# Kernel optimization log

Hardware: AMD Instinct MI355X
Metric: run time of the kernel (lower is better)

## Reference

```python
import jax, jax.numpy as jnp
import numpy as np

H = 768  # hidden size
L = 2    # num layers


def _lstm_layer(xs, ms, Wih, Whh, bih, bhh):
    """xs: [S,B,in], ms: [S,B,H] mask. Returns (outputs [S,B,H], (hT, cT)).
    PyTorch LSTMCell gate order: i, f, g, o. Zero initial state (module default),
    so the reset term init_hidden*(1-mask) is identically zero."""
    B = xs.shape[1]
    h0 = jnp.zeros((B, H), xs.dtype)
    c0 = jnp.zeros((B, H), xs.dtype)
    # Precompute input projections for all timesteps in one big GEMM.
    x_proj = jnp.einsum('sbi,gi->sbg', xs, Wih) + bih + bhh  # [S,B,4H]

    def step(carry, inp):
        h, c = carry
        xp, mt = inp
        gates = xp + h @ Whh.T  # [B,4H]
        i, f, g, o = jnp.split(gates, 4, axis=-1)
        i = jax.nn.sigmoid(i)
        f = jax.nn.sigmoid(f)
        g = jnp.tanh(g)
        o = jax.nn.sigmoid(o)
        c_next = (f * c + i * g)
        h_next = o * jnp.tanh(c_next)
        # mask-based state reset (h0=c0=0 -> pure multiply)
        h_next = h_next * mt
        c_next = c_next * mt
        return (h_next, c_next), h_next

    (hT, cT), outs = jax.lax.scan(step, (h0, c0), (x_proj, ms))
    return outs, (hT, cT)


def setup_inputs() -> dict:
    key = jax.random.key(0)
    ks = jax.random.split(key, 5)
    s = 0.05
    return {
        'x': jax.random.normal(ks[0], (64, 512, 768), jnp.float32),
        'mask': jnp.ones((64, 512), jnp.float32),
        'W_ih': jax.random.normal(ks[1], (L, 4 * H, 768), jnp.float32) * s,
        'W_hh': jax.random.normal(ks[2], (L, 4 * H, H), jnp.float32) * s,
        'b_ih': jax.random.normal(ks[3], (L, 4 * H), jnp.float32) * s,
        'b_hh': jax.random.normal(ks[4], (L, 4 * H), jnp.float32) * s,
    }


def reference(x, mask, W_ih, W_hh, b_ih, b_hh):
    # batch_first=True: transpose to [S,B,...]
    xs = jnp.transpose(x, (1, 0, 2))          # [S,B,in]
    ms = jnp.transpose(mask, (1, 0))[:, :, None]  # [S,B,1]
    ms = jnp.broadcast_to(ms, ms.shape[:2] + (H,))  # [S,B,H]
    hn, cn = [], []
    inp = xs
    for l in range(L):
        outs, (hT, cT) = _lstm_layer(inp, ms, W_ih[l], W_hh[l], b_ih[l], b_hh[l])
        hn.append(hT)
        cn.append(cT)
        inp = outs
    output = jnp.transpose(inp, (1, 0, 2))  # [B,S,H]
    return output, (jnp.stack(hn, 0), jnp.stack(cn, 0))
```

## Files before the change

### kernel.cpp

```cpp
#include <hip/hip_runtime.h>
#include <hip/hip_bf16.h>


#define HID 768
#define FH  3072
#define SEQ 512
#define BAT 64
#define GB  16
#define WPG 64
#define NWG 256
#define TPB 1024

typedef __attribute__((ext_vector_type(8))) __bf16 bf16x8;
typedef __attribute__((ext_vector_type(4))) float f32x4;
typedef unsigned int u32;
typedef unsigned long long u64;

__device__ __forceinline__ float sigm(float z) { return 1.f / (1.f + __expf(-z)); }
__device__ __forceinline__ float tanh_fast(float x) {
  float a = fabsf(x);
  float e = __expf(-2.f * a);
  float t = (1.f - e) / (1.f + e);
  return copysignf(t, x);
}
__device__ __forceinline__ unsigned short bfbits(__bf16 b) {
  union { __bf16 b; unsigned short s; } u; u.b = b; return u.s;
}
__device__ __forceinline__ __bf16 bits2bf(unsigned short s) {
  union { unsigned short s; __bf16 b; } u; u.s = s; return u.b;
}
__device__ __forceinline__ u32 packsplit(float v) {
  __bf16 h = (__bf16)v;
  __bf16 l = (__bf16)(v - (float)h);
  return ((u32)bfbits(h) << 16) | (u32)bfbits(l);
}
__device__ __forceinline__ void split8(const float* p, bf16x8& hi, bf16x8& lo) {
  const float4* q = (const float4*)p;
  float4 a = q[0], b = q[1];
  float v[8] = {a.x, a.y, a.z, a.w, b.x, b.y, b.z, b.w};
#pragma unroll
  for (int i = 0; i < 8; ++i) {
    __bf16 h = (__bf16)v[i];
    hi[i] = h;
    lo[i] = (__bf16)(v[i] - (float)h);
  }
}
__device__ __forceinline__ void unpack8(const u32 w[8], bf16x8& hi, bf16x8& lo) {
#pragma unroll
  for (int i = 0; i < 8; ++i) {
    hi[i] = bits2bf((unsigned short)(w[i] >> 16));
    lo[i] = bits2bf((unsigned short)(w[i] & 0xffffu));
  }
}
__device__ __forceinline__ bf16x8 q2b(uint4 q) {
  union { uint4 q; bf16x8 v; } u; u.q = q; return u.v;
}
__device__ __forceinline__ uint4 b2q(bf16x8 v) {
  union { bf16x8 v; uint4 q; } u; u.v = v; return u.q;
}

__global__ void pack_w(const float* __restrict__ Wih,
                       const float* __restrict__ Whh,
                       u32* __restrict__ wpk) {
  int g = blockIdx.x * blockDim.x + threadIdx.x;
  const int NT = 2 * 9216 * 64;
  if (g >= NT) return;
  int lane = g & 63;
  int sl = g >> 6;
  int region = sl / 9216;
  int sr = sl % 9216;
  int l15 = lane & 15, lhi = lane >> 4;
  int k, t, wid, layer;
  const float* W;
  if (region == 0) {
    int c  = sr % 8;
    t      = (sr / 8) % 3;
    int xw = (sr / 24) % 3;
    wid    = (sr / 72) % 64;
    layer  = sr / 4608;
    k = xw*256 + c*32 + lhi*8;
    W = Wih + (size_t)layer*FH*HID;
  } else {
    int c  = sr % 2;
    t      = (sr / 2) % 3;
    int j  = (sr / 6) % 12;
    wid    = (sr / 72) % 64;
    layer  = sr / 4608;
    k = j*64 + c*32 + lhi*8;
    W = Whh + (size_t)layer*FH*HID;
  }
  int row = (l15 & 3)*HID + wid*12 + t*4 + (l15 >> 2);
  bf16x8 hi, lo;
  split8(W + (size_t)row*HID + k, hi, lo);
  u32* dst = wpk + ((size_t)region*9216 + sr)*512 + lane*8;
  *(uint4*)dst       = b2q(hi);
  *(uint4*)(dst + 4) = b2q(lo);
}

#define MFMA16 __builtin_amdgcn_mfma_f32_16x16x32_bf16

template<int XFMT, int WRITE_OUT, int RING>
__attribute__((amdgpu_waves_per_eu(4, 4)))
__global__ void __launch_bounds__(TPB)
lstm_scan(const float* __restrict__ xf,
          const u32* __restrict__ xp,
          const float* __restrict__ mask,
          const u32* __restrict__ wipk,
          const u32* __restrict__ whpk,
          const float* __restrict__ bih,
          const float* __restrict__ bhh,
          u32* __restrict__ hdst,
          const u32* __restrict__ hsrc,
          float* __restrict__ out_f,
          float* __restrict__ hn, float* __restrict__ cn,
          int* __restrict__ flags)
{
  __shared__ f32x4 xring[4][3][3][64];
  __shared__ f32x4 hpart[12][3][64];
  __shared__ f32x4 padlds[512];

  const int wg  = blockIdx.x;
  const int grp = wg >> 6;
  const int wid = wg & 63;
  const int tid = threadIdx.x;
  const int wv  = tid >> 6;
  const int l   = tid & 63;
  const int l15 = l & 15;
  const int lhi = l >> 4;

  if ((int)blockIdx.x == -1) padlds[tid & 511] = hpart[0][0][0];

  const bool ish  = (wv < 12);
  const bool isxw = (wv >= 12 && wv < 15);
  const int j  = wv;
  const int xw = wv - 12;

  const int batch = grp*GB + l15;
  const u32* wbj = whpk + (size_t)(wid*12 + (ish  ? j  : 0))*6*512;
  const u32* wbx = wipk + (size_t)(wid*3  + (isxw ? xw : 0))*24*512;

  const int colO = wid*12 + (isxw ? xw : 0)*4 + lhi;
  float bias4[4] = {0.f, 0.f, 0.f, 0.f};
  if (isxw) {
#pragma unroll
    for (int r = 0; r < 4; ++r) bias4[r] = bih[r*HID + colO] + bhh[r*HID + colO];
  }
  const float* mrow = mask + batch*SEQ;
  int* gflags = flags + grp*WPG;
  float cstate = 0.f;

  auto xproj = [&](int sstep, int slot) {
    f32x4 a0{0.f,0.f,0.f,0.f}, a1{0.f,0.f,0.f,0.f}, a2{0.f,0.f,0.f,0.f};
#pragma unroll
    for (int c = 0; c < 8; ++c) {
      bf16x8 bhi, blo;
      if constexpr (XFMT == 0) {
        const float* src = xf + ((size_t)batch*SEQ + sstep)*HID + xw*256 + c*32 + lhi*8;
        split8(src, bhi, blo);
      } else {
        const u32* src = xp + ((size_t)sstep*BAT + batch)*HID + xw*256 + c*32 + lhi*8;
        uint4 A = *(const uint4*)src, B = *(const uint4*)(src + 4);
        u32 w[8] = {A.x,A.y,A.z,A.w,B.x,B.y,B.z,B.w};
        unpack8(w, bhi, blo);
      }
      {
        const uint4* wp = (const uint4*)(wbx + (size_t)(0*8 + c)*512 + l*8);
        bf16x8 Ah = q2b(wp[0]), Al = q2b(wp[1]);
        a0 = MFMA16(Ah, bhi, a0, 0,0,0); a0 = MFMA16(Al, bhi, a0, 0,0,0); a0 = MFMA16(Ah, blo, a0, 0,0,0);
      }
      {
        const uint4* wp = (const uint4*)(wbx + (size_t)(1*8 + c)*512 + l*8);
        bf16x8 Ah = q2b(wp[0]), Al = q2b(wp[1]);
        a1 = MFMA16(Ah, bhi, a1, 0,0,0); a1 = MFMA16(Al, bhi, a1, 0,0,0); a1 = MFMA16(Ah, blo, a1, 0,0,0);
      }
      {
        const uint4* wp = (const uint4*)(wbx + (size_t)(2*8 + c)*512 + l*8);
        bf16x8 Ah = q2b(wp[0]), Al = q2b(wp[1]);
        a2 = MFMA16(Ah, bhi, a2, 0,0,0); a2 = MFMA16(Al, bhi, a2, 0,0,0); a2 = MFMA16(Ah, blo, a2, 0,0,0);
      }
    }
    xring[slot][xw][0][l] = a0;
    xring[slot][xw][1][l] = a1;
    xring[slot][xw][2][l] = a2;
  };

  if (isxw) xproj(0, 0);
  __syncthreads();

#pragma unroll 1
  for (int s = 0; s < SEQ; ++s) {
    if (wv == 15 && s > 0) {
      while (true) {
        int v = __hip_atomic_load(gflags + l, __ATOMIC_RELAXED, __HIP_MEMORY_SCOPE_AGENT);
        if (__all(v >= s)) break;
        __builtin_amdgcn_s_sleep(1);
      }
    }
    __syncthreads();

    if (ish && s > 0) {
      f32x4 a0{0.f,0.f,0.f,0.f}, a1{0.f,0.f,0.f,0.f}, a2{0.f,0.f,0.f,0.f};
#pragma unroll
      for (int c = 0; c < 2; ++c) {
        u32 w[8];
        if constexpr (RING) {
          const u64* sp = (const u64*)(hsrc + ((size_t)((s-1)&1)*BAT + batch)*HID + j*64 + c*32 + lhi*8);
          u64 qa = __hip_atomic_load(sp,   __ATOMIC_RELAXED, __HIP_MEMORY_SCOPE_AGENT);
          u64 qb = __hip_atomic_load(sp+1, __ATOMIC_RELAXED, __HIP_MEMORY_SCOPE_AGENT);
          u64 qc = __hip_atomic_load(sp+2, __ATOMIC_RELAXED, __HIP_MEMORY_SCOPE_AGENT);
          u64 qd = __hip_atomic_load(sp+3, __ATOMIC_RELAXED, __HIP_MEMORY_SCOPE_AGENT);
          w[0]=(u32)qa; w[1]=(u32)(qa>>32); w[2]=(u32)qb; w[3]=(u32)(qb>>32);
          w[4]=(u32)qc; w[5]=(u32)(qc>>32); w[6]=(u32)qd; w[7]=(u32)(qd>>32);
        } else {
          const u32* sp = hsrc + ((size_t)(s-1)*BAT + batch)*HID + j*64 + c*32 + lhi*8;
          uint4 A = *(const uint4*)sp, B = *(const uint4*)(sp + 4);
          w[0]=A.x; w[1]=A.y; w[2]=A.z; w[3]=A.w;
          w[4]=B.x; w[5]=B.y; w[6]=B.z; w[7]=B.w;
        }
        bf16x8 bhi, blo;
        unpack8(w, bhi, blo);
        {
          const uint4* wp = (const uint4*)(wbj + (size_t)(0*2 + c)*512 + l*8);
          bf16x8 Ah = q2b(wp[0]), Al = q2b(wp[1]);
          a0 = MFMA16(Ah, bhi, a0, 0,0,0); a0 = MFMA16(Al, bhi, a0, 0,0,0); a0 = MFMA16(Ah, blo, a0, 0,0,0);
        }
        {
          const uint4* wp = (const uint4*)(wbj + (size_t)(1*2 + c)*512 + l*8);
          bf16x8 Ah = q2b(wp[0]), Al = q2b(wp[1]);
          a1 = MFMA16(Ah, bhi, a1, 0,0,0); a1 = MFMA16(Al, bhi, a1, 0,0,0); a1 = MFMA16(Ah, blo, a1, 0,0,0);
        }
        {
          const uint4* wp = (const uint4*)(wbj + (size_t)(2*2 + c)*512 + l*8);
          bf16x8 Ah = q2b(wp[0]), Al = q2b(wp[1]);
          a2 = MFMA16(Ah, bhi, a2, 0,0,0); a2 = MFMA16(Al, bhi, a2, 0,0,0); a2 = MFMA16(Ah, blo, a2, 0,0,0);
        }
      }
      hpart[j][0][l] = a0;
      hpart[j][1][l] = a1;
      hpart[j][2][l] = a2;
    }
    if (isxw && s + 1 < SEQ) xproj(s + 1, (s + 1) & 3);
    __syncthreads();

    if (isxw) {
      f32x4 z = xring[s & 3][0][xw][l] + xring[s & 3][1][xw][l] + xring[s & 3][2][xw][l];
      if (s > 0) {
#pragma unroll
        for (int jj = 0; jj < 12; ++jj) z = z + hpart[jj][xw][l];
      }
      float zi = z[0] + bias4[0], zf = z[1] + bias4[1];
      float zg = z[2] + bias4[2], zo = z[3] + bias4[3];
      float iv = sigm(zi), fv = sigm(zf), gv = tanh_fast(zg), ov = sigm(zo);
      float c  = fv*cstate + iv*gv;
      float hv = ov * tanh_fast(c);
      float m  = mrow[s];
      hv *= m; c *= m; cstate = c;

      u32 hw = packsplit(hv);
      size_t wrow = RING ? ((size_t)(s & 1)*BAT + batch)*HID + colO
                         : ((size_t)s*BAT + batch)*HID + colO;
      __hip_atomic_store(hdst + wrow, hw,
                         __ATOMIC_RELAXED, __HIP_MEMORY_SCOPE_AGENT);
      if constexpr (WRITE_OUT) {
        __builtin_nontemporal_store(hv, out_f + ((size_t)batch*SEQ + s)*HID + colO);
      }
      if (s == SEQ - 1) {
        hn[batch*HID + colO] = hv;
        cn[batch*HID + colO] = c;
      }
      asm volatile("s_waitcnt vmcnt(0)" ::: "memory");
    }
    __syncthreads();
    if (tid == 0)
      __hip_atomic_store(gflags + wid, s + 1,
                         __ATOMIC_RELAXED, __HIP_MEMORY_SCOPE_AGENT);
  }
}

extern "C" void kernel_launch(void* const* d_in, const int* in_sizes, int n_in,
                              void* d_out, int out_size, void* d_ws, size_t ws_size,
                              hipStream_t stream) {
  const float* x    = (const float*)d_in[0];
  const float* mask = (const float*)d_in[1];
  const float* Wih  = (const float*)d_in[2];
  const float* Whh  = (const float*)d_in[3];
  const float* bih  = (const float*)d_in[4];
  const float* bhh  = (const float*)d_in[5];
  float* out = (float*)d_out;

  char* ws = (char*)d_ws;
  const size_t WPK_B   = (size_t)2*9216*512*4;
  const size_t STREAM_B = (size_t)SEQ*BAT*HID*4;
  const size_t RING_B  = (size_t)2*BAT*HID*4;

  u32* wpk = (u32*)ws;
  u32* opk = (u32*)(ws + WPK_B);
  const bool big = ws_size >= WPK_B + 2*STREAM_B + 4096;
  u32* h1  = (u32*)(ws + WPK_B + STREAM_B);
  int* flags = big ? (int*)(ws + WPK_B + 2*STREAM_B)
                   : (int*)(ws + WPK_B + STREAM_B + RING_B);

  (void)hipMemsetAsync(flags, 0, 2*NWG*sizeof(int), stream);
  pack_w<<<4608, 256, 0, stream>>>(Wih, Whh, wpk);

  float* hn = out + 25165824;
  float* cn = out + 25165824 + 98304;

  const u32* wipk0 = wpk;
  const u32* wipk1 = wpk + (size_t)4608*512;
  const u32* whpk0 = wpk + (size_t)9216*512;
  const u32* whpk1 = wpk + (size_t)13824*512;

  lstm_scan<0, 0, 0><<<dim3(NWG), dim3(TPB), 0, stream>>>(
      x, nullptr, mask, wipk0, whpk0, bih, bhh,
      opk, opk, nullptr, hn, cn, flags);

  if (big) {
    lstm_scan<1, 1, 0><<<dim3(NWG), dim3(TPB), 0, stream>>>(
        nullptr, opk, mask, wipk1, whpk1, bih + FH, bhh + FH,
        h1, h1, out, hn + 49152, cn + 49152, flags + NWG);
  } else {
    lstm_scan<1, 1, 1><<<dim3(NWG), dim3(TPB), 0, stream>>>(
        nullptr, opk, mask, wipk1, whpk1, bih + FH, bhh + FH,
        h1, h1, out, hn + 49152, cn + 49152, flags + NWG);
  }
}
```

Measured before the change: 13.76 ms.

## Replace flag-poll barrier with per-step arrival counters polled by hidden waves

The old scheme had a dedicated wave poll 64 per-workgroup flags, then ran a block barrier at the top of every timestep, and published progress after a second barrier. Now each group keeps a per-timestep global counter that the three gate-writing waves bump through an LDS tally. Only the recurrent-matmul waves spin on the previous step's counter, which removes one block barrier per step and its fan-in latency. hpart is double-buffered and the input projection is prefetched two steps ahead so the gate waves can overlap with the next step's recurrent work. The cost is more LDS, a larger zeroed counter array, and more delicate ordering, especially in the two-slot ring mode.

```diff
diff --git a/kernel.cpp b/kernel.cpp
--- a/kernel.cpp
+++ b/kernel.cpp
@@ -7,7 +7,6 @@
 #define SEQ 512
 #define BAT 64
 #define GB  16
-#define WPG 64
 #define NWG 256
 #define TPB 1024
 
@@ -70,11 +69,10 @@
   int region = sl / 9216;
   int sr = sl % 9216;
   int l15 = lane & 15, lhi = lane >> 4;
-  int k, t, wid, layer;
+  int k, wid, layer;
   const float* W;
   if (region == 0) {
     int c  = sr % 8;
-    t      = (sr / 8) % 3;
     int xw = (sr / 24) % 3;
     wid    = (sr / 72) % 64;
     layer  = sr / 4608;
@@ -82,13 +80,13 @@
     W = Wih + (size_t)layer*FH*HID;
   } else {
     int c  = sr % 2;
-    t      = (sr / 2) % 3;
     int j  = (sr / 6) % 12;
     wid    = (sr / 72) % 64;
     layer  = sr / 4608;
     k = j*64 + c*32 + lhi*8;
     W = Whh + (size_t)layer*FH*HID;
   }
+  int t = (region == 0) ? (sr / 8) % 3 : (sr / 2) % 3;
   int row = (l15 & 3)*HID + wid*12 + t*4 + (l15 >> 2);
   bf16x8 hi, lo;
   split8(W + (size_t)row*HID + k, hi, lo);
@@ -113,11 +111,11 @@
           const u32* __restrict__ hsrc,
           float* __restrict__ out_f,
           float* __restrict__ hn, float* __restrict__ cn,
-          int* __restrict__ flags)
+          int* __restrict__ cnt)
 {
   __shared__ f32x4 xring[4][3][3][64];
-  __shared__ f32x4 hpart[12][3][64];
-  __shared__ f32x4 padlds[512];
+  __shared__ f32x4 hpart[2][12][3][64];
+  __shared__ int   lfin[SEQ];
 
   const int wg  = blockIdx.x;
   const int grp = wg >> 6;
@@ -128,8 +126,6 @@
   const int l15 = l & 15;
   const int lhi = l >> 4;
 
-  if ((int)blockIdx.x == -1) padlds[tid & 511] = hpart[0][0][0];
-
   const bool ish  = (wv < 12);
   const bool isxw = (wv >= 12 && wv < 15);
   const int j  = wv;
@@ -146,8 +142,10 @@
     for (int r = 0; r < 4; ++r) bias4[r] = bih[r*HID + colO] + bhh[r*HID + colO];
   }
   const float* mrow = mask + batch*SEQ;
-  int* gflags = flags + grp*WPG;
+  int* gcnt = cnt + grp*SEQ;
   float cstate = 0.f;
+
+  for (int i = tid; i < SEQ; i += TPB) lfin[i] = 0;
 
   auto xproj = [&](int sstep, int slot) {
     f32x4 a0{0.f,0.f,0.f,0.f}, a1{0.f,0.f,0.f,0.f}, a2{0.f,0.f,0.f,0.f};
@@ -184,21 +182,14 @@
     xring[slot][xw][2][l] = a2;
   };
 
-  if (isxw) xproj(0, 0);
-  __syncthreads();
+  if (isxw) { xproj(0, 0); xproj(1, 1); }
 
 #pragma unroll 1
   for (int s = 0; s < SEQ; ++s) {
-    if (wv == 15 && s > 0) {
-      while (true) {
-        int v = __hip_atomic_load(gflags + l, __ATOMIC_RELAXED, __HIP_MEMORY_SCOPE_AGENT);
-        if (__all(v >= s)) break;
-        __builtin_amdgcn_s_sleep(1);
-      }
-    }
-    __syncthreads();
-
     if (ish && s > 0) {
+      const int* cp = gcnt + (s - 1);
+      while (__hip_atomic_load(cp, __ATOMIC_RELAXED, __HIP_MEMORY_SCOPE_AGENT) < 64)
+        __builtin_amdgcn_s_sleep(2);
       f32x4 a0{0.f,0.f,0.f,0.f}, a1{0.f,0.f,0.f,0.f}, a2{0.f,0.f,0.f,0.f};
 #pragma unroll
       for (int c = 0; c < 2; ++c) {
@@ -235,18 +226,18 @@
           a2 = MFMA16(Ah, bhi, a2, 0,0,0); a2 = MFMA16(Al, bhi, a2, 0,0,0); a2 = MFMA16(Ah, blo, a2, 0,0,0);
         }
       }
-      hpart[j][0][l] = a0;
-      hpart[j][1][l] = a1;
-      hpart[j][2][l] = a2;
+      hpart[s & 1][j][0][l] = a0;
+      hpart[s & 1][j][1][l] = a1;
+      hpart[s & 1][j][2][l] = a2;
     }
-    if (isxw && s + 1 < SEQ) xproj(s + 1, (s + 1) & 3);
+    if (isxw && s + 2 < SEQ) xproj(s + 2, (s + 2) & 3);
     __syncthreads();
 
     if (isxw) {
       f32x4 z = xring[s & 3][0][xw][l] + xring[s & 3][1][xw][l] + xring[s & 3][2][xw][l];
       if (s > 0) {
 #pragma unroll
-        for (int jj = 0; jj < 12; ++jj) z = z + hpart[jj][xw][l];
+        for (int jj = 0; jj < 12; ++jj) z = z + hpart[s & 1][jj][xw][l];
       }
       float zi = z[0] + bias4[0], zf = z[1] + bias4[1];
       float zg = z[2] + bias4[2], zo = z[3] + bias4[3];
@@ -269,11 +260,13 @@
         cn[batch*HID + colO] = c;
       }
       asm volatile("s_waitcnt vmcnt(0)" ::: "memory");
+      if (l == 0) {
+        int old = atomicAdd(&lfin[s], 1);
+        if (old == 2)
+          __hip_atomic_fetch_add(gcnt + s, 1,
+                                 __ATOMIC_RELAXED, __HIP_MEMORY_SCOPE_AGENT);
+      }
     }
-    __syncthreads();
-    if (tid == 0)
-      __hip_atomic_store(gflags + wid, s + 1,
-                         __ATOMIC_RELAXED, __HIP_MEMORY_SCOPE_AGENT);
   }
 }
 
@@ -295,12 +288,12 @@
 
   u32* wpk = (u32*)ws;
   u32* opk = (u32*)(ws + WPK_B);
-  const bool big = ws_size >= WPK_B + 2*STREAM_B + 4096;
+  const bool big = ws_size >= WPK_B + 2*STREAM_B + 65536;
   u32* h1  = (u32*)(ws + WPK_B + STREAM_B);
-  int* flags = big ? (int*)(ws + WPK_B + 2*STREAM_B)
-                   : (int*)(ws + WPK_B + STREAM_B + RING_B);
-
-  (void)hipMemsetAsync(flags, 0, 2*NWG*sizeof(int), stream);
+  int* cnt = big ? (int*)(ws + WPK_B + 2*STREAM_B)
+                 : (int*)(ws + WPK_B + STREAM_B + RING_B);
+
+  (void)hipMemsetAsync(cnt, 0, 2*4*SEQ*sizeof(int), stream);
   pack_w<<<4608, 256, 0, stream>>>(Wih, Whh, wpk);
 
   float* hn = out + 25165824;
@@ -313,15 +306,15 @@
 
   lstm_scan<0, 0, 0><<<dim3(NWG), dim3(TPB), 0, stream>>>(
       x, nullptr, mask, wipk0, whpk0, bih, bhh,
-      opk, opk, nullptr, hn, cn, flags);
+      opk, opk, nullptr, hn, cn, cnt);
 
   if (big) {
     lstm_scan<1, 1, 0><<<dim3(NWG), dim3(TPB), 0, stream>>>(
         nullptr, opk, mask, wipk1, whpk1, bih + FH, bhh + FH,
-        h1, h1, out, hn + 49152, cn + 49152, flags + NWG);
+        h1, h1, out, hn + 49152, cn + 49152, cnt + 4*SEQ);
   } else {
     lstm_scan<1, 1, 1><<<dim3(NWG), dim3(TPB), 0, stream>>>(
         nullptr, opk, mask, wipk1, whpk1, bih + FH, bhh + FH,
-        h1, h1, out, hn + 49152, cn + 49152, flags + NWG);
-  }
-}
+        h1, h1, out, hn + 49152, cn + 49152, cnt + 4*SEQ);
+  }
+}
```

Result: slower. 15.16 ms (+10.2%).

## Split input projection into segmented GEMM kernels and keep Whh in registers

Applied to the files above, without the earlier changes.

Moves the per-step input projection out of the persistent scan kernel into a separate batched GEMM over 64-step segments. The scan runs segment by segment and carries cell state through global memory between launches. Recurrent Whh fragments now stay in registers instead of being reloaded every step. Step completion is signalled per workgroup through an LDS counter instead of a block-wide barrier. The cost is 16 extra kernel launches and a round trip of the projection results through global memory, in exchange for a shorter serial critical path per step.

```diff
diff --git a/kernel.cpp b/kernel.cpp
--- a/kernel.cpp
+++ b/kernel.cpp
@@ -7,9 +7,11 @@
 #define SEQ 512
 #define BAT 64
 #define GB  16
-#define WPG 64
+#define SSEG 64
+#define SEGS 8
 #define NWG 256
-#define TPB 1024
+#define STPB 960
+#define GTPB 768
 
 typedef __attribute__((ext_vector_type(8))) __bf16 bf16x8;
 typedef __attribute__((ext_vector_type(4))) float f32x4;
@@ -33,6 +35,10 @@
   __bf16 h = (__bf16)v;
   __bf16 l = (__bf16)(v - (float)h);
   return ((u32)bfbits(h) << 16) | (u32)bfbits(l);
+}
+__device__ __forceinline__ float unpackf(u32 w) {
+  return (float)bits2bf((unsigned short)(w >> 16)) +
+         (float)bits2bf((unsigned short)(w & 0xffffu));
 }
 __device__ __forceinline__ void split8(const float* p, bf16x8& hi, bf16x8& lo) {
   const float4* q = (const float4*)p;
@@ -73,12 +79,12 @@
   int k, t, wid, layer;
   const float* W;
   if (region == 0) {
-    int c  = sr % 8;
-    t      = (sr / 8) % 3;
-    int xw = (sr / 24) % 3;
+    int c  = sr % 6;
+    int ks = (sr / 6) % 4;
+    t      = (sr / 24) % 3;
     wid    = (sr / 72) % 64;
     layer  = sr / 4608;
-    k = xw*256 + c*32 + lhi*8;
+    k = ks*192 + c*32 + lhi*8;
     W = Wih + (size_t)layer*FH*HID;
   } else {
     int c  = sr % 2;
@@ -99,25 +105,101 @@
 
 #define MFMA16 __builtin_amdgcn_mfma_f32_16x16x32_bf16
 
-template<int XFMT, int WRITE_OUT, int RING>
-__attribute__((amdgpu_waves_per_eu(4, 4)))
-__global__ void __launch_bounds__(TPB)
-lstm_scan(const float* __restrict__ xf,
-          const u32* __restrict__ xp,
+template<int XFMT>
+__global__ void __launch_bounds__(GTPB)
+xproj_gemm(const float* __restrict__ xf,
+           const u32* __restrict__ xp,
+           const u32* __restrict__ wih_pk,
+           u32* __restrict__ xpk,
+           int s0)
+{
+  __shared__ f32x4 part[3][4][4][64];
+
+  const int wg  = blockIdx.x;
+  const int sq  = wg & 3;
+  const int wid = (wg >> 2) & 63;
+  const int grp = wg >> 8;
+  const int tid = threadIdx.x;
+  const int wv  = tid >> 6;
+  const int l   = tid & 63;
+  const int l15 = l & 15;
+  const int lhi = l >> 4;
+  const int t   = wv >> 2;
+  const int ks  = wv & 3;
+
+  const int batch = grp*GB + l15;
+  const u32* wb = wih_pk + (((size_t)(wid*3 + t)*4 + ks)*6)*512;
+
+  uint4 wa[12];
+#pragma unroll
+  for (int c = 0; c < 6; ++c) {
+    const uint4* wp = (const uint4*)(wb + (size_t)c*512 + l*8);
+    wa[c*2]   = wp[0];
+    wa[c*2+1] = wp[1];
+  }
+
+#pragma unroll 1
+  for (int i0 = 0; i0 < 16; i0 += 4) {
+    f32x4 acc[4];
+#pragma unroll
+    for (int i = 0; i < 4; ++i) acc[i] = f32x4{0.f, 0.f, 0.f, 0.f};
+#pragma unroll
+    for (int c = 0; c < 6; ++c) {
+      int k = ks*192 + c*32 + lhi*8;
+      bf16x8 Ah = q2b(wa[c*2]), Al = q2b(wa[c*2+1]);
+#pragma unroll
+      for (int i = 0; i < 4; ++i) {
+        int sg = s0 + sq*16 + i0 + i;
+        bf16x8 bhi, blo;
+        if constexpr (XFMT == 0) {
+          split8(xf + ((size_t)batch*SEQ + sg)*HID + k, bhi, blo);
+        } else {
+          const u32* sp = xp + ((size_t)sg*BAT + batch)*HID + k;
+          uint4 A = *(const uint4*)sp, B = *(const uint4*)(sp + 4);
+          u32 w[8] = {A.x, A.y, A.z, A.w, B.x, B.y, B.z, B.w};
+          unpack8(w, bhi, blo);
+        }
+        acc[i] = MFMA16(Ah, bhi, acc[i], 0, 0, 0);
+        acc[i] = MFMA16(Al, bhi, acc[i], 0, 0, 0);
+        acc[i] = MFMA16(Ah, blo, acc[i], 0, 0, 0);
+      }
+    }
+#pragma unroll
+    for (int i = 0; i < 4; ++i) part[t][ks][i][l] = acc[i];
+    __syncthreads();
+    if (ks == 0) {
+#pragma unroll
+      for (int i = 0; i < 4; ++i) {
+        f32x4 z = part[t][0][i][l] + part[t][1][i][l]
+                + part[t][2][i][l] + part[t][3][i][l];
+        int soff = sq*16 + i0 + i;
+        u32* dst = xpk + ((size_t)((soff*4 + grp)*64 + wid)*3 + t)*256 + l*4;
+        *(uint4*)dst = make_uint4(packsplit(z[0]), packsplit(z[1]),
+                                  packsplit(z[2]), packsplit(z[3]));
+      }
+    }
+    __syncthreads();
+  }
+}
+
+template<int LAYER>
+__global__ void __launch_bounds__(STPB)
+lstm_scan(const u32* __restrict__ xpk,
           const float* __restrict__ mask,
-          const u32* __restrict__ wipk,
-          const u32* __restrict__ whpk,
+          const u32* __restrict__ whh_pk,
           const float* __restrict__ bih,
           const float* __restrict__ bhh,
           u32* __restrict__ hdst,
           const u32* __restrict__ hsrc,
           float* __restrict__ out_f,
           float* __restrict__ hn, float* __restrict__ cn,
-          int* __restrict__ flags)
+          float* __restrict__ cs,
+          int* __restrict__ flags,
+          int s0)
 {
-  __shared__ f32x4 xring[4][3][3][64];
   __shared__ f32x4 hpart[12][3][64];
-  __shared__ f32x4 padlds[512];
+  __shared__ int lfin[SSEG];
+  __shared__ f32x4 pad_lds[2816];
 
   const int wg  = blockIdx.x;
   const int grp = wg >> 6;
@@ -128,72 +210,51 @@
   const int l15 = l & 15;
   const int lhi = l >> 4;
 
-  if ((int)blockIdx.x == -1) padlds[tid & 511] = hpart[0][0][0];
-
-  const bool ish  = (wv < 12);
-  const bool isxw = (wv >= 12 && wv < 15);
-  const int j  = wv;
-  const int xw = wv - 12;
+  if ((int)blockIdx.x == -1) pad_lds[tid & 2047] = hpart[0][0][0];
+
+  const bool ish   = (wv < 12);
+  const bool isfin = (wv >= 12);
+  const int  t     = wv - 12;
 
   const int batch = grp*GB + l15;
-  const u32* wbj = whpk + (size_t)(wid*12 + (ish  ? j  : 0))*6*512;
-  const u32* wbx = wipk + (size_t)(wid*3  + (isxw ? xw : 0))*24*512;
-
-  const int colO = wid*12 + (isxw ? xw : 0)*4 + lhi;
+  int* gflags = flags + grp*64;
+
+  for (int i = tid; i < SSEG; i += STPB) lfin[i] = 0;
+
+  uint4 wa[12];
+  if (ish) {
+    const u32* wbj = whh_pk + (size_t)(wid*12 + wv)*6*512;
+#pragma unroll
+    for (int tc = 0; tc < 6; ++tc) {
+      const uint4* wp = (const uint4*)(wbj + (size_t)tc*512 + l*8);
+      wa[tc*2]   = wp[0];
+      wa[tc*2+1] = wp[1];
+    }
+  }
+
+  const int colO = wid*12 + (isfin ? t : 0)*4 + lhi;
   float bias4[4] = {0.f, 0.f, 0.f, 0.f};
-  if (isxw) {
+  float cstate = 0.f;
+  if (isfin) {
 #pragma unroll
     for (int r = 0; r < 4; ++r) bias4[r] = bih[r*HID + colO] + bhh[r*HID + colO];
+    if (s0 > 0) cstate = cs[batch*HID + colO];
   }
   const float* mrow = mask + batch*SEQ;
-  int* gflags = flags + grp*WPG;
-  float cstate = 0.f;
-
-  auto xproj = [&](int sstep, int slot) {
-    f32x4 a0{0.f,0.f,0.f,0.f}, a1{0.f,0.f,0.f,0.f}, a2{0.f,0.f,0.f,0.f};
-#pragma unroll
-    for (int c = 0; c < 8; ++c) {
-      bf16x8 bhi, blo;
-      if constexpr (XFMT == 0) {
-        const float* src = xf + ((size_t)batch*SEQ + sstep)*HID + xw*256 + c*32 + lhi*8;
-        split8(src, bhi, blo);
-      } else {
-        const u32* src = xp + ((size_t)sstep*BAT + batch)*HID + xw*256 + c*32 + lhi*8;
-        uint4 A = *(const uint4*)src, B = *(const uint4*)(src + 4);
-        u32 w[8] = {A.x,A.y,A.z,A.w,B.x,B.y,B.z,B.w};
-        unpack8(w, bhi, blo);
-      }
-      {
-        const uint4* wp = (const uint4*)(wbx + (size_t)(0*8 + c)*512 + l*8);
-        bf16x8 Ah = q2b(wp[0]), Al = q2b(wp[1]);
-        a0 = MFMA16(Ah, bhi, a0, 0,0,0); a0 = MFMA16(Al, bhi, a0, 0,0,0); a0 = MFMA16(Ah, blo, a0, 0,0,0);
-      }
-      {
-        const uint4* wp = (const uint4*)(wbx + (size_t)(1*8 + c)*512 + l*8);
-        bf16x8 Ah = q2b(wp[0]), Al = q2b(wp[1]);
-        a1 = MFMA16(Ah, bhi, a1, 0,0,0); a1 = MFMA16(Al, bhi, a1, 0,0,0); a1 = MFMA16(Ah, blo, a1, 0,0,0);
-      }
-      {
-        const uint4* wp = (const uint4*)(wbx + (size_t)(2*8 + c)*512 + l*8);
-        bf16x8 Ah = q2b(wp[0]), Al = q2b(wp[1]);
-        a2 = MFMA16(Ah, bhi, a2, 0,0,0); a2 = MFMA16(Al, bhi, a2, 0,0,0); a2 = MFMA16(Ah, blo, a2, 0,0,0);
-      }
-    }
-    xring[slot][xw][0][l] = a0;
-    xring[slot][xw][1][l] = a1;
-    xring[slot][xw][2][l] = a2;
-  };
-
-  if (isxw) xproj(0, 0);
+
   __syncthreads();
 
 #pragma unroll 1
-  for (int s = 0; s < SEQ; ++s) {
-    if (wv == 15 && s > 0) {
-      while (true) {
-        int v = __hip_atomic_load(gflags + l, __ATOMIC_RELAXED, __HIP_MEMORY_SCOPE_AGENT);
-        if (__all(v >= s)) break;
-        __builtin_amdgcn_s_sleep(1);
+  for (int s = s0; s < s0 + SSEG; ++s) {
+    uint4 xq = make_uint4(0, 0, 0, 0);
+    if (isfin) {
+      xq = *(const uint4*)(xpk + ((size_t)(((s - s0)*4 + grp)*64 + wid)*3 + t)*256 + l*4);
+      if (t == 0 && s > 0) {
+        while (true) {
+          int v = __hip_atomic_load(gflags + l, __ATOMIC_RELAXED, __HIP_MEMORY_SCOPE_AGENT);
+          if (__all(v >= s)) break;
+          __builtin_amdgcn_s_sleep(1);
+        }
       }
     }
     __syncthreads();
@@ -202,9 +263,10 @@
       f32x4 a0{0.f,0.f,0.f,0.f}, a1{0.f,0.f,0.f,0.f}, a2{0.f,0.f,0.f,0.f};
 #pragma unroll
       for (int c = 0; c < 2; ++c) {
+        int k = wv*64 + c*32 + lhi*8;
         u32 w[8];
-        if constexpr (RING) {
-          const u64* sp = (const u64*)(hsrc + ((size_t)((s-1)&1)*BAT + batch)*HID + j*64 + c*32 + lhi*8);
+        if constexpr (LAYER == 1) {
+          const u64* sp = (const u64*)(hsrc + ((size_t)((s-1)&1)*BAT + batch)*HID + k);
           u64 qa = __hip_atomic_load(sp,   __ATOMIC_RELAXED, __HIP_MEMORY_SCOPE_AGENT);
           u64 qb = __hip_atomic_load(sp+1, __ATOMIC_RELAXED, __HIP_MEMORY_SCOPE_AGENT);
           u64 qc = __hip_atomic_load(sp+2, __ATOMIC_RELAXED, __HIP_MEMORY_SCOPE_AGENT);
@@ -212,7 +274,7 @@
           w[0]=(u32)qa; w[1]=(u32)(qa>>32); w[2]=(u32)qb; w[3]=(u32)(qb>>32);
           w[4]=(u32)qc; w[5]=(u32)(qc>>32); w[6]=(u32)qd; w[7]=(u32)(qd>>32);
         } else {
-          const u32* sp = hsrc + ((size_t)(s-1)*BAT + batch)*HID + j*64 + c*32 + lhi*8;
+          const u32* sp = hsrc + ((size_t)(s-1)*BAT + batch)*HID + k;
           uint4 A = *(const uint4*)sp, B = *(const uint4*)(sp + 4);
           w[0]=A.x; w[1]=A.y; w[2]=A.z; w[3]=A.w;
           w[4]=B.x; w[5]=B.y; w[6]=B.z; w[7]=B.w;
@@ -220,33 +282,29 @@
         bf16x8 bhi, blo;
         unpack8(w, bhi, blo);
         {
-          const uint4* wp = (const uint4*)(wbj + (size_t)(0*2 + c)*512 + l*8);
-          bf16x8 Ah = q2b(wp[0]), Al = q2b(wp[1]);
+          bf16x8 Ah = q2b(wa[(0*2+c)*2]), Al = q2b(wa[(0*2+c)*2+1]);
           a0 = MFMA16(Ah, bhi, a0, 0,0,0); a0 = MFMA16(Al, bhi, a0, 0,0,0); a0 = MFMA16(Ah, blo, a0, 0,0,0);
         }
         {
-          const uint4* wp = (const uint4*)(wbj + (size_t)(1*2 + c)*512 + l*8);
-          bf16x8 Ah = q2b(wp[0]), Al = q2b(wp[1]);
+          bf16x8 Ah = q2b(wa[(1*2+c)*2]), Al = q2b(wa[(1*2+c)*2+1]);
           a1 = MFMA16(Ah, bhi, a1, 0,0,0); a1 = MFMA16(Al, bhi, a1, 0,0,0); a1 = MFMA16(Ah, blo, a1, 0,0,0);
         }
         {
-          const uint4* wp = (const uint4*)(wbj + (size_t)(2*2 + c)*512 + l*8);
-          bf16x8 Ah = q2b(wp[0]), Al = q2b(wp[1]);
+          bf16x8 Ah = q2b(wa[(2*2+c)*2]), Al = q2b(wa[(2*2+c)*2+1]);
           a2 = MFMA16(Ah, bhi, a2, 0,0,0); a2 = MFMA16(Al, bhi, a2, 0,0,0); a2 = MFMA16(Ah, blo, a2, 0,0,0);
         }
       }
-      hpart[j][0][l] = a0;
-      hpart[j][1][l] = a1;
-      hpart[j][2][l] = a2;
-    }
-    if (isxw && s + 1 < SEQ) xproj(s + 1, (s + 1) & 3);
+      hpart[wv][0][l] = a0;
+      hpart[wv][1][l] = a1;
+      hpart[wv][2][l] = a2;
+    }
     __syncthreads();
 
-    if (isxw) {
-      f32x4 z = xring[s & 3][0][xw][l] + xring[s & 3][1][xw][l] + xring[s & 3][2][xw][l];
+    if (isfin) {
+      f32x4 z = f32x4{unpackf(xq.x), unpackf(xq.y), unpackf(xq.z), unpackf(xq.w)};
       if (s > 0) {
 #pragma unroll
-        for (int jj = 0; jj < 12; ++jj) z = z + hpart[jj][xw][l];
+        for (int j = 0; j < 12; ++j) z = z + hpart[j][t][l];
       }
       float zi = z[0] + bias4[0], zf = z[1] + bias4[1];
       float zg = z[2] + bias4[2], zo = z[3] + bias4[3];
@@ -257,23 +315,26 @@
       hv *= m; c *= m; cstate = c;
 
       u32 hw = packsplit(hv);
-      size_t wrow = RING ? ((size_t)(s & 1)*BAT + batch)*HID + colO
-                         : ((size_t)s*BAT + batch)*HID + colO;
+      size_t wrow = (LAYER == 1) ? ((size_t)(s & 1)*BAT + batch)*HID + colO
+                                 : ((size_t)s*BAT + batch)*HID + colO;
       __hip_atomic_store(hdst + wrow, hw,
                          __ATOMIC_RELAXED, __HIP_MEMORY_SCOPE_AGENT);
-      if constexpr (WRITE_OUT) {
+      if constexpr (LAYER == 1) {
         __builtin_nontemporal_store(hv, out_f + ((size_t)batch*SEQ + s)*HID + colO);
       }
       if (s == SEQ - 1) {
         hn[batch*HID + colO] = hv;
         cn[batch*HID + colO] = c;
       }
+      if (s == s0 + SSEG - 1) cs[batch*HID + colO] = cstate;
       asm volatile("s_waitcnt vmcnt(0)" ::: "memory");
-    }
-    __syncthreads();
-    if (tid == 0)
-      __hip_atomic_store(gflags + wid, s + 1,
-                         __ATOMIC_RELAXED, __HIP_MEMORY_SCOPE_AGENT);
+      if (l == 0) {
+        int old = atomicAdd(&lfin[s - s0], 1);
+        if (old == 2)
+          __hip_atomic_store(gflags + wid, s + 1,
+                             __ATOMIC_RELAXED, __HIP_MEMORY_SCOPE_AGENT);
+      }
+    }
   }
 }
 
@@ -289,39 +350,44 @@
   float* out = (float*)d_out;
 
   char* ws = (char*)d_ws;
-  const size_t WPK_B   = (size_t)2*9216*512*4;
-  const size_t STREAM_B = (size_t)SEQ*BAT*HID*4;
-  const size_t RING_B  = (size_t)2*BAT*HID*4;
-
-  u32* wpk = (u32*)ws;
-  u32* opk = (u32*)(ws + WPK_B);
-  const bool big = ws_size >= WPK_B + 2*STREAM_B + 4096;
-  u32* h1  = (u32*)(ws + WPK_B + STREAM_B);
-  int* flags = big ? (int*)(ws + WPK_B + 2*STREAM_B)
-                   : (int*)(ws + WPK_B + STREAM_B + RING_B);
-
-  (void)hipMemsetAsync(flags, 0, 2*NWG*sizeof(int), stream);
+  const size_t WPK_B  = (size_t)2*9216*512*4;
+  const size_t XPK_B  = (size_t)SSEG*BAT*FH*4;
+  const size_t STRM_B = (size_t)SEQ*BAT*HID*4;
+  const size_t RING_B = (size_t)2*BAT*HID*4;
+  const size_t CS_B   = (size_t)2*BAT*HID*4;
+
+  u32* wpk  = (u32*)ws;
+  u32* xpk  = (u32*)(ws + WPK_B);
+  u32* opk  = (u32*)(ws + WPK_B + XPK_B);
+  u32* ring = (u32*)(ws + WPK_B + XPK_B + STRM_B);
+  float* cs = (float*)(ws + WPK_B + XPK_B + STRM_B + RING_B);
+  int* flags = (int*)(ws + WPK_B + XPK_B + STRM_B + RING_B + CS_B);
+
+  (void)hipMemsetAsync(flags, 0, 2*4*64*sizeof(int), stream);
   pack_w<<<4608, 256, 0, stream>>>(Wih, Whh, wpk);
 
   float* hn = out + 25165824;
   float* cn = out + 25165824 + 98304;
 
-  const u32* wipk0 = wpk;
-  const u32* wipk1 = wpk + (size_t)4608*512;
-  const u32* whpk0 = wpk + (size_t)9216*512;
-  const u32* whpk1 = wpk + (size_t)13824*512;
-
-  lstm_scan<0, 0, 0><<<dim3(NWG), dim3(TPB), 0, stream>>>(
-      x, nullptr, mask, wipk0, whpk0, bih, bhh,
-      opk, opk, nullptr, hn, cn, flags);
-
-  if (big) {
-    lstm_scan<1, 1, 0><<<dim3(NWG), dim3(TPB), 0, stream>>>(
-        nullptr, opk, mask, wipk1, whpk1, bih + FH, bhh + FH,
-        h1, h1, out, hn + 49152, cn + 49152, flags + NWG);
-  } else {
-    lstm_scan<1, 1, 1><<<dim3(NWG), dim3(TPB), 0, stream>>>(
-        nullptr, opk, mask, wipk1, whpk1, bih + FH, bhh + FH,
-        h1, h1, out, hn + 49152, cn + 49152, flags + NWG);
-  }
-}
+  const u32* wih0 = wpk;
+  const u32* wih1 = wpk + (size_t)4608*512;
+  const u32* whh0 = wpk + (size_t)9216*512;
+  const u32* whh1 = wpk + (size_t)13824*512;
+
+  for (int seg = 0; seg < SEGS; ++seg) {
+    int s0 = seg * SSEG;
+    xproj_gemm<0><<<dim3(1024), dim3(GTPB), 0, stream>>>(
+        x, nullptr, wih0, xpk, s0);
+    lstm_scan<0><<<dim3(NWG), dim3(STPB), 0, stream>>>(
+        xpk, mask, whh0, bih, bhh,
+        opk, opk, nullptr, hn, cn, cs, flags, s0);
+  }
+  for (int seg = 0; seg < SEGS; ++seg) {
+    int s0 = seg * SSEG;
+    xproj_gemm<1><<<dim3(1024), dim3(GTPB), 0, stream>>>(
+        nullptr, opk, wih1, xpk, s0);
+    lstm_scan<1><<<dim3(NWG), dim3(STPB), 0, stream>>>(
+        xpk, mask, whh1, bih + FH, bhh + FH,
+        ring, ring, out, hn + 49152, cn + 49152, cs + 49152, flags + 4*64, s0);
+  }
+}
```

Result: faster. 13.12 ms (-4.6%).
